# Kernel tuning notes

Measured on AMD Instinct MI355X. Metric: run time of the kernel, lower is better.

Reference implementation:

```python
import jax, jax.numpy as jnp
import numpy as np

B = 4096
FLAT = 3 * 10 * 10 * 40  # 12000

def setup_inputs() -> dict:
    key = jax.random.key(0)
    ks = jax.random.split(key, 9)
    s = lambda fan_in: 1.0 / np.sqrt(fan_in)
    return {
        "x": jax.random.normal(ks[0], (B, 3, 10, 10, 40), dtype=jnp.float32),
        "conv_w": jax.random.normal(ks[1], (1, 3), dtype=jnp.float32) * s(3),   # Conv3d(3,1,k=1), no bias
        "F_w": jax.random.normal(ks[2], (3, 1), dtype=jnp.float32) * s(1),      # Conv3d(1,3,k=1), no bias
        "w1": jax.random.normal(ks[3], (4096, FLAT), dtype=jnp.float32) * s(FLAT),
        "b1": jnp.zeros((4096,), dtype=jnp.float32),
        "w2": jax.random.normal(ks[4], (512, 4096), dtype=jnp.float32) * s(4096),
        "b2": jnp.zeros((512,), dtype=jnp.float32),
        "w3": jax.random.normal(ks[5], (3, 512), dtype=jnp.float32) * s(512),
        "b3": jnp.zeros((3,), dtype=jnp.float32),
    }

def reference(x, conv_w, F_w, w1, b1, w2, b2, w3, b3):
    # Adaptive avg pools (input is exactly [B,3,10,10,40], so pools are plain means)
    xd = x.mean(axis=(3, 4), keepdims=True).transpose(0, 1, 4, 3, 2)  # [B,3,1,1,10]
    xh = x.mean(axis=(2, 4), keepdims=True).transpose(0, 1, 2, 4, 3)  # [B,3,1,1,10]
    xw = x.mean(axis=(2, 3), keepdims=True)                           # [B,3,1,1,40]
    cat = jnp.concatenate([xd, xh, xw], axis=4)                       # [B,3,1,1,60]
    y = jax.nn.relu(jnp.einsum('oc,bcdhw->bodhw', conv_w, cat))       # [B,1,1,1,60]
    sh = y[..., 10:20]  # [B,1,1,1,10]
    sw = y[..., 20:]    # [B,1,1,1,40]
    # NOTE: faithful to original code, which feeds x_h into the x_d branch.
    gd = jax.nn.sigmoid(jnp.einsum('oc,bcdhw->bodhw', F_w, sh.transpose(0, 1, 4, 3, 2)))  # [B,3,10,1,1]
    gh = jax.nn.sigmoid(jnp.einsum('oc,bcdhw->bodhw', F_w, sh.transpose(0, 1, 2, 4, 3)))  # [B,3,1,10,1]
    gw = jax.nn.sigmoid(jnp.einsum('oc,bcdhw->bodhw', F_w, sw))                            # [B,3,1,1,40]
    z = x * gd * gh * gw                      # [B,3,10,10,40]
    z = z.reshape(z.shape[0], -1)             # [B,12000]
    z = jax.nn.relu(z @ w1.T + b1)
    z = jax.nn.relu(z @ w2.T + b2)
    z = z @ w3.T + b3                          # [B,3]
    norm = jnp.linalg.norm(z, axis=1, keepdims=True)
    return z / jnp.maximum(norm, 1e-12)
```

## Files before the change

kernel.cpp:

```cpp
#include <hip/hip_runtime.h>
#include <hip/hip_fp16.h>

typedef _Float16 f16_t;
typedef __attribute__((ext_vector_type(8))) _Float16 f16x8;
typedef __attribute__((ext_vector_type(4))) _Float16 f16x4;
typedef __attribute__((ext_vector_type(4))) float f32x4;

__device__ __forceinline__ void gload_lds16(const void* g, void* lds) {
    __builtin_amdgcn_global_load_lds(
        (const __attribute__((address_space(1))) unsigned int*)g,
        (__attribute__((address_space(3))) unsigned int*)lds,
        16, 0, 0);
}

__device__ __forceinline__ float sigmoidf_(float v) {
    return 1.0f / (1.0f + expf(-v));
}

__global__ __launch_bounds__(256) void gate_kernel(
    const float* __restrict__ x, const float* __restrict__ conv_w,
    const float* __restrict__ F_w, f16_t* __restrict__ G) {
    __shared__ alignas(16) float xs[12000];
    __shared__ float part[240];
    __shared__ float mW[120];
    __shared__ float sv[10];
    __shared__ float tv[40];
    __shared__ float gsv[3][10];
    __shared__ float gwv[3][40];

    const int t = threadIdx.x;
    const long b = blockIdx.x;
    const float4* xp = (const float4*)(x + b * 12000);
    float4* xs4 = (float4*)xs;
    for (int i = t; i < 3000; i += 256) xs4[i] = xp[i];
    __syncthreads();

    if (t < 240) {
        int c = t / 80, h = (t % 80) / 8, g = t % 8;
        const float* p = xs + c * 4000 + h * 40 + g * 5;
        float s = 0.f;
        #pragma unroll
        for (int d = 0; d < 10; ++d)
            #pragma unroll
            for (int j = 0; j < 5; ++j) s += p[d * 400 + j];
        part[t] = s;
    }
    if (t < 120) {
        int c = t / 40, w = t % 40;
        const float* p = xs + c * 4000 + w;
        float s = 0.f;
        #pragma unroll
        for (int d = 0; d < 10; ++d)
            #pragma unroll
            for (int h = 0; h < 10; ++h) s += p[d * 400 + h * 40];
        mW[t] = s;
    }
    __syncthreads();
    if (t < 10) {
        float a = 0.f;
        #pragma unroll
        for (int c = 0; c < 3; ++c) {
            float m = 0.f;
            #pragma unroll
            for (int g = 0; g < 8; ++g) m += part[c * 80 + t * 8 + g];
            a += conv_w[c] * (m * (1.f / 400.f));
        }
        sv[t] = fmaxf(a, 0.f);
    }
    if (t < 40) {
        float a = 0.f;
        #pragma unroll
        for (int c = 0; c < 3; ++c) a += conv_w[c] * (mW[c * 40 + t] * (1.f / 100.f));
        tv[t] = fmaxf(a, 0.f);
    }
    __syncthreads();
    if (t < 30) { int c = t / 10, k = t % 10; gsv[c][k] = sigmoidf_(F_w[c] * sv[k]); }
    if (t < 120) { int c = t / 40, w = t % 40; gwv[c][w] = sigmoidf_(F_w[c] * tv[w]); }
    __syncthreads();

    f16x4* Gp = (f16x4*)(G + b * 12032);
    for (int i = t; i < 3000; i += 256) {
        int flat = i * 4;
        int c = flat / 4000, rem = flat % 4000;
        int d = rem / 400, rem2 = rem % 400;
        int h = rem2 / 40, w0 = rem2 % 40;
        float gdh = gsv[c][d] * gsv[c][h];
        float4 v = xs4[i];
        f16x4 o;
        o[0] = (f16_t)(v.x * gdh * gwv[c][w0 + 0]);
        o[1] = (f16_t)(v.y * gdh * gwv[c][w0 + 1]);
        o[2] = (f16_t)(v.z * gdh * gwv[c][w0 + 2]);
        o[3] = (f16_t)(v.w * gdh * gwv[c][w0 + 3]);
        Gp[i] = o;
    }
    if (t < 8) Gp[3000 + t] = (f16x4){};
}

__global__ __launch_bounds__(256) void cvt_f16_pad(
    const float* __restrict__ in, f16_t* __restrict__ out) {
    const long r = blockIdx.x;
    const float4* ip = (const float4*)(in + r * 12000);
    f16x4* op = (f16x4*)(out + r * 12032);
    for (int i = threadIdx.x; i < 3000; i += 256) {
        float4 v = ip[i];
        f16x4 o;
        o[0] = (f16_t)v.x; o[1] = (f16_t)v.y; o[2] = (f16_t)v.z; o[3] = (f16_t)v.w;
        op[i] = o;
    }
    if (threadIdx.x < 8) op[3000 + threadIdx.x] = (f16x4){};
}

__global__ __launch_bounds__(256) void cvt_f16(
    const float* __restrict__ in, f16_t* __restrict__ out, long n4) {
    long stride = (long)gridDim.x * 256;
    for (long i = (long)blockIdx.x * 256 + threadIdx.x; i < n4; i += stride) {
        float4 v = ((const float4*)in)[i];
        f16x4 o;
        o[0] = (f16_t)v.x; o[1] = (f16_t)v.y; o[2] = (f16_t)v.z; o[3] = (f16_t)v.w;
        ((f16x4*)out)[i] = o;
    }
}

__global__ __launch_bounds__(512, 2) void gemm1_kphase(
    const f16_t* __restrict__ A, const f16_t* __restrict__ B,
    const float* __restrict__ bias, f16_t* __restrict__ C,
    int M, int N, int K2, int NT) {
    __shared__ alignas(16) f16_t lds[65536];
    const int t = threadIdx.x;
    const int lane = t & 63, w = t >> 6;
    const int wr = w >> 2, wc = w & 3;
    const int l15 = lane & 15, lg = lane >> 4;
    const long tileM = (long)blockIdx.y * 256;
    const long tileN = (long)blockIdx.x * 256;
    const long lK2 = K2;

    const int srow = t >> 2;
    const int gs8 = ((t & 3) ^ ((t >> 3) & 3)) * 8;
    auto stage_half = [&](int dst, int ph, long kk) {
        f16_t* dA = lds + dst * 32768 + ph * 8192;
        f16_t* dB = dA + 16384;
        gload_lds16(A + (tileM + srow) * lK2 + kk + gs8, dA + t * 8);
        gload_lds16(A + (tileM + srow + 128) * lK2 + kk + gs8, dA + 4096 + t * 8);
        gload_lds16(B + (tileN + srow) * lK2 + kk + gs8, dB + t * 8);
        gload_lds16(B + (tileN + srow + 128) * lK2 + kk + gs8, dB + 4096 + t * 8);
    };

    const int sl8 = (lg ^ ((l15 >> 1) & 3)) * 8;

    f32x4 acc[8][4] = {};

    stage_half(0, 0, 0);
    stage_half(0, 1, 32);
    asm volatile("s_waitcnt vmcnt(4)" ::: "memory");
    __builtin_amdgcn_s_barrier();

    for (int kt = 0; kt < NT; ++kt) {
        const int c = kt & 1;
        const f16_t* bufc = lds + c * 32768;
        const bool more = (kt + 1 < NT);
        #pragma unroll
        for (int ph = 0; ph < 2; ++ph) {
            f16x8 af[2][4], bf[2][2];
            #pragma unroll
            for (int qm = 0; qm < 2; ++qm)
                #pragma unroll
                for (int mf = 0; mf < 4; ++mf)
                    af[qm][mf] = *(const f16x8*)(bufc + ph * 8192 +
                        (wr * 128 + qm * 64 + mf * 16 + l15) * 32 + sl8);
            #pragma unroll
            for (int qn = 0; qn < 2; ++qn)
                #pragma unroll
                for (int nf = 0; nf < 2; ++nf)
                    bf[qn][nf] = *(const f16x8*)(bufc + 16384 + ph * 8192 +
                        (wc * 64 + qn * 32 + nf * 16 + l15) * 32 + sl8);
            if (more) stage_half(c ^ 1, ph, (long)(kt + 1) * 64 + ph * 32);
            __builtin_amdgcn_s_setprio(1);
            #pragma unroll
            for (int qn = 0; qn < 2; ++qn)
                #pragma unroll
                for (int nf = 0; nf < 2; ++nf)
                    #pragma unroll
                    for (int qm = 0; qm < 2; ++qm)
                        #pragma unroll
                        for (int mf = 0; mf < 4; ++mf)
                            acc[qm * 4 + mf][qn * 2 + nf] =
                                __builtin_amdgcn_mfma_f32_16x16x32_f16(
                                    af[qm][mf], bf[qn][nf],
                                    acc[qm * 4 + mf][qn * 2 + nf], 0, 0, 0);
            __builtin_amdgcn_s_setprio(0);
            if (more) asm volatile("s_waitcnt vmcnt(4)" ::: "memory");
            else      asm volatile("s_waitcnt vmcnt(0)" ::: "memory");
            __builtin_amdgcn_s_barrier();
        }
    }

    const long rowC0 = tileM + wr * 128 + lg * 4;
    const long colC0 = tileN + wc * 64 + l15;
    #pragma unroll
    for (int ni = 0; ni < 4; ++ni) {
        long col = colC0 + ni * 16;
        float bia = bias[col];
        #pragma unroll
        for (int mi = 0; mi < 8; ++mi) {
            #pragma unroll
            for (int r = 0; r < 4; ++r) {
                long row = rowC0 + mi * 16 + r;
                float o = fmaxf(acc[mi][ni][r] + bia, 0.f);
                C[row * (long)N + col] = (f16_t)o;
            }
        }
    }
}

__global__ __launch_bounds__(256) void gemm2_nt(
    const f16_t* __restrict__ A, const f16_t* __restrict__ B,
    const float* __restrict__ bias, float* __restrict__ Cf,
    int M, int N, int K) {
    __shared__ alignas(16) f16_t As[64 * 32];
    __shared__ alignas(16) f16_t Bs[128 * 32];
    const int t = threadIdx.x;
    const int lane = t & 63, wid = t >> 6;
    const int wr = wid >> 1, wc = wid & 1;
    const int l15 = lane & 15, lg = lane >> 4;
    const long rowA0 = (long)blockIdx.y * 64;
    const long colB0 = (long)blockIdx.x * 128;

    const int eA = t * 8;
    const int rA = eA >> 5, kA = eA & 31;
    const int eB0 = t * 8;
    const int rB0 = eB0 >> 5, kB0 = eB0 & 31;
    const int eB1 = eB0 + 2048;
    const int rB1 = eB1 >> 5, kB1 = eB1 & 31;

    int aoff[2], boff[4];
    #pragma unroll
    for (int m = 0; m < 2; ++m) aoff[m] = (wr * 32 + m * 16 + l15) * 32 + lg * 8;
    #pragma unroll
    for (int n = 0; n < 4; ++n) boff[n] = (wc * 64 + n * 16 + l15) * 32 + lg * 8;

    f32x4 acc[2][4] = {};

    for (int kk = 0; kk < K; kk += 32) {
        __syncthreads();
        gload_lds16(A + (rowA0 + rA) * (long)K + kk + kA, As + eA);
        gload_lds16(B + (colB0 + rB0) * (long)K + kk + kB0, Bs + eB0);
        gload_lds16(B + (colB0 + rB1) * (long)K + kk + kB1, Bs + eB1);
        __syncthreads();

        f16x8 af[2], bfv[4];
        #pragma unroll
        for (int m = 0; m < 2; ++m) af[m] = *(const f16x8*)(As + aoff[m]);
        #pragma unroll
        for (int n = 0; n < 4; ++n) bfv[n] = *(const f16x8*)(Bs + boff[n]);
        #pragma unroll
        for (int m = 0; m < 2; ++m)
            #pragma unroll
            for (int n = 0; n < 4; ++n)
                acc[m][n] = __builtin_amdgcn_mfma_f32_16x16x32_f16(
                    af[m], bfv[n], acc[m][n], 0, 0, 0);
    }

    const long rowC0 = rowA0 + wr * 32 + lg * 4;
    const long colC0 = colB0 + wc * 64 + l15;
    #pragma unroll
    for (int n = 0; n < 4; ++n) {
        long col = colC0 + n * 16;
        float bia = bias[col];
        #pragma unroll
        for (int m = 0; m < 2; ++m) {
            #pragma unroll
            for (int r = 0; r < 4; ++r) {
                long row = rowC0 + m * 16 + r;
                float o = fmaxf(acc[m][n][r] + bia, 0.f);
                Cf[row * (long)N + col] = o;
            }
        }
    }
}

__global__ __launch_bounds__(256) void head_kernel(
    const float* __restrict__ z2, const float* __restrict__ w3,
    const float* __restrict__ b3, float* __restrict__ out) {
    const int lane = threadIdx.x & 63, wid = threadIdx.x >> 6;
    const long b = (long)blockIdx.x * 4 + wid;
    const float4* zp = (const float4*)(z2 + b * 512);
    float4 z0 = zp[lane * 2], z1 = zp[lane * 2 + 1];
    float d[3];
    #pragma unroll
    for (int o = 0; o < 3; ++o) {
        const float4* wp = (const float4*)(w3 + o * 512);
        float4 a0 = wp[lane * 2], a1 = wp[lane * 2 + 1];
        d[o] = z0.x * a0.x + z0.y * a0.y + z0.z * a0.z + z0.w * a0.w +
               z1.x * a1.x + z1.y * a1.y + z1.z * a1.z + z1.w * a1.w;
    }
    #pragma unroll
    for (int o = 0; o < 3; ++o)
        #pragma unroll
        for (int off = 1; off < 64; off <<= 1) d[o] += __shfl_xor(d[o], off);
    float d0 = d[0] + b3[0], d1 = d[1] + b3[1], d2 = d[2] + b3[2];
    float nrm = fmaxf(sqrtf(d0 * d0 + d1 * d1 + d2 * d2), 1e-12f);
    if (lane < 3) {
        float v = (lane == 0) ? d0 : (lane == 1) ? d1 : d2;
        out[b * 3 + lane] = v / nrm;
    }
}

extern "C" void kernel_launch(void* const* d_in, const int* in_sizes, int n_in,
                              void* d_out, int out_size, void* d_ws, size_t ws_size,
                              hipStream_t stream) {
    const float* x      = (const float*)d_in[0];
    const float* conv_w = (const float*)d_in[1];
    const float* F_w    = (const float*)d_in[2];
    const float* w1     = (const float*)d_in[3];
    const float* b1     = (const float*)d_in[4];
    const float* w2     = (const float*)d_in[5];
    const float* b2     = (const float*)d_in[6];
    const float* w3     = (const float*)d_in[7];
    const float* b3     = (const float*)d_in[8];
    float* out = (float*)d_out;

    char* ws = (char*)d_ws;
    f16_t* G   = (f16_t*)(ws);
    f16_t* w1h = (f16_t*)(ws + 98566144L);
    f16_t* z1  = (f16_t*)(ws + 197132288L);
    f16_t* w2h = (f16_t*)(ws + 230686720L);
    float* z2  = (float*)(ws);

    gate_kernel<<<4096, 256, 0, stream>>>(x, conv_w, F_w, G);
    cvt_f16_pad<<<4096, 256, 0, stream>>>(w1, w1h);
    cvt_f16<<<512, 256, 0, stream>>>(w2, w2h, 524288L);
    gemm1_kphase<<<dim3(16, 16), 512, 0, stream>>>(G, w1h, b1, z1, 4096, 4096, 12032, 188);
    gemm2_nt<<<dim3(4, 64), 256, 0, stream>>>(z1, w2h, b2, z2, 4096, 512, 4096);
    head_kernel<<<1024, 256, 0, stream>>>(z2, w3, b3, out);
}
```

Baseline: 552.1 us.

## Software-pipeline LDS fragment reads with double-buffered register fragments

Restructures the GEMM main loop so the LDS fragment reads for the next K-half are issued before the MFMA block of the current half. Two register fragment sets alternate, which hides LDS read latency behind matrix instructions. This raises register pressure because two fragment sets are live at once. The barrier and waitcnt placement also changes, so correctness depends on the new ordering of global_load_lds completions relative to reads.

```diff
diff --git a/kernel.cpp b/kernel.cpp
--- a/kernel.cpp
+++ b/kernel.cpp
@@ -147,51 +147,62 @@
 
     const int sl8 = (lg ^ ((l15 >> 1) & 3)) * 8;
 
+    auto readFrags = [&](f16x8 (&fa)[2][4], f16x8 (&fb)[4],
+                         const f16_t* bufc, int ph) {
+        const f16_t* pa = bufc + ph * 8192;
+        const f16_t* pb = bufc + 16384 + ph * 8192;
+        #pragma unroll
+        for (int qm = 0; qm < 2; ++qm)
+            #pragma unroll
+            for (int mf = 0; mf < 4; ++mf)
+                fa[qm][mf] = *(const f16x8*)(pa +
+                    (wr * 128 + qm * 64 + mf * 16 + l15) * 32 + sl8);
+        #pragma unroll
+        for (int n = 0; n < 4; ++n)
+            fb[n] = *(const f16x8*)(pb + (wc * 64 + n * 16 + l15) * 32 + sl8);
+    };
+
     f32x4 acc[8][4] = {};
+    auto mfmaSet = [&](f16x8 (&fa)[2][4], f16x8 (&fb)[4]) {
+        __builtin_amdgcn_s_setprio(1);
+        #pragma unroll
+        for (int n = 0; n < 4; ++n)
+            #pragma unroll
+            for (int qm = 0; qm < 2; ++qm)
+                #pragma unroll
+                for (int mf = 0; mf < 4; ++mf)
+                    acc[qm * 4 + mf][n] = __builtin_amdgcn_mfma_f32_16x16x32_f16(
+                        fa[qm][mf], fb[n], acc[qm * 4 + mf][n], 0, 0, 0);
+        __builtin_amdgcn_s_setprio(0);
+    };
+
+    f16x8 aX[2][4], bX[4];
+    f16x8 aY[2][4], bY[4];
 
     stage_half(0, 0, 0);
     stage_half(0, 1, 32);
     asm volatile("s_waitcnt vmcnt(4)" ::: "memory");
     __builtin_amdgcn_s_barrier();
+    readFrags(aX, bX, lds, 0);
 
     for (int kt = 0; kt < NT; ++kt) {
         const int c = kt & 1;
         const f16_t* bufc = lds + c * 32768;
+        const f16_t* bufn = lds + (c ^ 1) * 32768;
         const bool more = (kt + 1 < NT);
-        #pragma unroll
-        for (int ph = 0; ph < 2; ++ph) {
-            f16x8 af[2][4], bf[2][2];
-            #pragma unroll
-            for (int qm = 0; qm < 2; ++qm)
-                #pragma unroll
-                for (int mf = 0; mf < 4; ++mf)
-                    af[qm][mf] = *(const f16x8*)(bufc + ph * 8192 +
-                        (wr * 128 + qm * 64 + mf * 16 + l15) * 32 + sl8);
-            #pragma unroll
-            for (int qn = 0; qn < 2; ++qn)
-                #pragma unroll
-                for (int nf = 0; nf < 2; ++nf)
-                    bf[qn][nf] = *(const f16x8*)(bufc + 16384 + ph * 8192 +
-                        (wc * 64 + qn * 32 + nf * 16 + l15) * 32 + sl8);
-            if (more) stage_half(c ^ 1, ph, (long)(kt + 1) * 64 + ph * 32);
-            __builtin_amdgcn_s_setprio(1);
-            #pragma unroll
-            for (int qn = 0; qn < 2; ++qn)
-                #pragma unroll
-                for (int nf = 0; nf < 2; ++nf)
-                    #pragma unroll
-                    for (int qm = 0; qm < 2; ++qm)
-                        #pragma unroll
-                        for (int mf = 0; mf < 4; ++mf)
-                            acc[qm * 4 + mf][qn * 2 + nf] =
-                                __builtin_amdgcn_mfma_f32_16x16x32_f16(
-                                    af[qm][mf], bf[qn][nf],
-                                    acc[qm * 4 + mf][qn * 2 + nf], 0, 0, 0);
-            __builtin_amdgcn_s_setprio(0);
-            if (more) asm volatile("s_waitcnt vmcnt(4)" ::: "memory");
-            else      asm volatile("s_waitcnt vmcnt(0)" ::: "memory");
+        if (more) stage_half(c ^ 1, 0, (long)(kt + 1) * 64);
+        if (more) asm volatile("s_waitcnt vmcnt(4)" ::: "memory");
+        else      asm volatile("s_waitcnt vmcnt(0)" ::: "memory");
+        __builtin_amdgcn_s_barrier();
+        readFrags(aY, bY, bufc, 1);
+        mfmaSet(aX, bX);
+        if (more) {
+            stage_half(c ^ 1, 1, (long)(kt + 1) * 64 + 32);
+            asm volatile("s_waitcnt vmcnt(4)" ::: "memory");
             __builtin_amdgcn_s_barrier();
+            readFrags(aX, bX, bufn, 0);
         }
+        mfmaSet(aY, bY);
     }
 
     const long rowC0 = tileM + wr * 128 + lg * 4;
```

Result: no change. 554.7 us (+0.5%).
